# Optimization experiments

Hardware: AMD Instinct MI355X
Metric: run time of the kernel (lower is better)

## Reference

```python
import jax, jax.numpy as jnp
import numpy as np
from jax import lax

B, C, H, W = 8, 512, 16, 16
Di, N, R, K = 1024, 16, 32, 4  # d_inner, d_state, dt_rank, num scan directions
EPS = 1e-5


def _ln(x, g, b):
    mu = x.mean(-1, keepdims=True)
    var = ((x - mu) ** 2).mean(-1, keepdims=True)
    return (x - mu) * lax.rsqrt(var + EPS) * g + b


def _ss2d_core(xc, x_proj_w, dt_w, dt_b, A_logs, Ds):
    # xc: (b, Di, H, W) after depthwise conv + SiLU. 4-direction selective scan.
    b = xc.shape[0]
    L = H * W
    x_flat = xc.reshape(b, Di, L)
    x_wh = xc.transpose(0, 1, 3, 2).reshape(b, Di, L)
    x_hwwh = jnp.stack([x_flat, x_wh], 1)                  # (b,2,Di,L)
    xs = jnp.concatenate([x_hwwh, x_hwwh[..., ::-1]], 1)   # (b,K,Di,L)
    x_dbl = jnp.einsum('bkdl,kcd->bkcl', xs, x_proj_w)     # (b,K,R+2N,L)
    dts, Bs, Cs = x_dbl[:, :, :R], x_dbl[:, :, R:R + N], x_dbl[:, :, R + N:]
    dts = jnp.einsum('bkrl,kdr->bkdl', dts, dt_w)
    delta = jax.nn.softplus(dts + dt_b[None, :, :, None])  # (b,K,Di,L)
    A = -jnp.exp(A_logs).reshape(K, Di, N)                 # (K,Di,N)

    def step(h, inp):
        d, u, Bl, Cl = inp  # d,u:(b,K,Di)  Bl,Cl:(b,K,N)
        h = jnp.exp(d[..., None] * A) * h + (d * u)[..., None] * Bl[:, :, None, :]
        yl = jnp.einsum('bkdn,bkn->bkd', h, Cl)
        return h, yl

    inps = (delta.transpose(3, 0, 1, 2), xs.transpose(3, 0, 1, 2),
            Bs.transpose(3, 0, 1, 2), Cs.transpose(3, 0, 1, 2))
    h0 = jnp.zeros((b, K, Di, N), xc.dtype)
    _, ys = lax.scan(step, h0, inps)                       # (L,b,K,Di)
    ys = ys.transpose(1, 2, 3, 0) + xs * Ds.reshape(1, K, Di, 1)  # + D*u skip
    inv = ys[:, 2:4, :, ::-1]
    wh = ys[:, 1].reshape(b, Di, W, H).transpose(0, 1, 3, 2).reshape(b, Di, L)
    invwh = inv[:, 1].reshape(b, Di, W, H).transpose(0, 1, 3, 2).reshape(b, Di, L)
    y = ys[:, 0] + inv[:, 0] + wh + invwh                  # (b,Di,L)
    return y.transpose(0, 2, 1).reshape(b, H, W, Di)


def _conv_ffn(x, ffn_conv_w, bn_g, bn_b, bn_mean, bn_var, fc1_w, fc2_w):
    x = lax.conv_general_dilated(x, ffn_conv_w, (1, 1), [(1, 1), (1, 1)],
                                 dimension_numbers=('NCHW', 'OIHW', 'NCHW'))
    x = ((x - bn_mean[:, None, None]) * lax.rsqrt(bn_var + EPS)[:, None, None]
         * bn_g[:, None, None] + bn_b[:, None, None])
    x = jnp.clip(x, 0.0, 6.0)                              # ReLU6
    x = jnp.einsum('bchw,oc->bohw', x, fc1_w)              # 1x1 conv fc1
    x = jax.nn.gelu(x, approximate=False)
    return jnp.einsum('bchw,oc->bohw', x, fc2_w)           # 1x1 conv fc2


def _forward(x, y, ln1_g, ln1_b, in_proj_w, conv_w, conv_b, x_proj_w, dt_w,
             dt_b, A_logs, Ds, out_norm_g, out_norm_b, out_proj_w, ffn_conv_w,
             bn_g, bn_b, bn_mean, bn_var, fc1_w, fc2_w, lin1_w, lin1_b,
             lin2_w, lin2_b):
    # --- VSSBlock: LN -> SS2D -> residual ---
    x1 = x.transpose(0, 2, 3, 1)                           # (B,H,W,C)
    xn = _ln(x1, ln1_g, ln1_b)
    xz = jnp.einsum('bhwc,oc->bhwo', xn, in_proj_w)        # in_proj (no bias)
    xa, z = xz[..., :Di], xz[..., Di:]
    xc = xa.transpose(0, 3, 1, 2)                          # (B,Di,H,W)
    xc = lax.conv_general_dilated(xc, conv_w, (1, 1), [(1, 1), (1, 1)],
                                  feature_group_count=Di,
                                  dimension_numbers=('NCHW', 'OIHW', 'NCHW'))
    xc = jax.nn.silu(xc + conv_b[:, None, None])
    yc = _ss2d_core(xc, x_proj_w, dt_w, dt_b, A_logs, Ds)  # (B,H,W,Di)
    yc = _ln(yc, out_norm_g, out_norm_b) * jax.nn.silu(z)
    vss = x1 + jnp.einsum('bhwd,od->bhwo', yc, out_proj_w)
    # --- ConvFFN ---
    xm = _conv_ffn(vss.transpose(0, 3, 1, 2), ffn_conv_w, bn_g, bn_b, bn_mean,
                   bn_var, fc1_w, fc2_w)                   # (B,C,H,W)
    # --- channel attention: both pools are AdaptiveAvgPool2d(1), so max==avg ---
    pooled = y.mean(axis=(2, 3))                           # (B,C)
    lin = jax.nn.relu(pooled @ lin1_w.T + lin1_b) @ lin2_w.T + lin2_b
    gate = jax.nn.sigmoid(2.0 * lin)                       # linear_max + linear_avg
    return gate[:, :, None, None] * xm


def setup_inputs() -> dict:
    key = jax.random.key(0)
    ks = jax.random.split(key, 16)
    n = lambda i, shape, s=0.05: jax.random.normal(ks[i], shape, jnp.float32) * s
    return {
        'x': n(0, (B, C, H, W), 1.0),
        'y': n(1, (B, C, H, W), 1.0),
        'ln1_g': jnp.ones((C,), jnp.float32), 'ln1_b': jnp.zeros((C,), jnp.float32),
        'in_proj_w': n(2, (2 * Di, C)),
        'conv_w': n(3, (Di, 1, 3, 3), 0.2), 'conv_b': jnp.zeros((Di,), jnp.float32),
        'x_proj_w': n(4, (K, R + 2 * N, Di)),
        'dt_w': n(5, (K, Di, R), 0.1), 'dt_b': n(6, (K, Di), 0.1),
        'A_logs': n(7, (K * Di, N), 0.1), 'Ds': jnp.ones((K * Di,), jnp.float32),
        'out_norm_g': jnp.ones((Di,), jnp.float32), 'out_norm_b': jnp.zeros((Di,), jnp.float32),
        'out_proj_w': n(8, (C, Di)),
        'ffn_conv_w': n(9, (C, C, 3, 3)),
        'bn_g': jnp.ones((C,), jnp.float32), 'bn_b': jnp.zeros((C,), jnp.float32),
        'bn_mean': jnp.zeros((C,), jnp.float32), 'bn_var': jnp.ones((C,), jnp.float32),
        'fc1_w': n(10, (C, C)), 'fc2_w': n(11, (C, C)),
        'lin1_w': n(12, (C // 2, C)), 'lin1_b': jnp.zeros((C // 2,), jnp.float32),
        'lin2_w': n(13, (C, C // 2)), 'lin2_b': jnp.zeros((C,), jnp.float32),
    }


def reference(x, y, ln1_g, ln1_b, in_proj_w, conv_w, conv_b, x_proj_w, dt_w,
              dt_b, A_logs, Ds, out_norm_g, out_norm_b, out_proj_w, ffn_conv_w,
              bn_g, bn_b, bn_mean, bn_var, fc1_w, fc2_w, lin1_w, lin1_b,
              lin2_w, lin2_b):
    return _forward(x, y, ln1_g, ln1_b, in_proj_w, conv_w, conv_b, x_proj_w,
                    dt_w, dt_b, A_logs, Ds, out_norm_g, out_norm_b, out_proj_w,
                    ffn_conv_w, bn_g, bn_b, bn_mean, bn_var, fc1_w, fc2_w,
                    lin1_w, lin1_b, lin2_w, lin2_b)
```

## Files before the change

### kernel.cpp

```cpp
#include <hip/hip_runtime.h>
#include <hip/hip_bf16.h>
#include <math.h>

#define DEV_INLINE __device__ __forceinline__

constexpr int B_ = 8, C_ = 512, L_ = 256;
constexpr float EPS_ = 1e-5f;

typedef __attribute__((ext_vector_type(8))) short bf16x8;
typedef __attribute__((ext_vector_type(4))) float f32x4;

DEV_INLINE int lmap1(int l) { return ((l & 15) << 4) | (l >> 4); }
DEV_INLINE float sigmoidf_(float x) { return 1.f / (1.f + __expf(-x)); }
DEV_INLINE float siluf_(float x) { return x * sigmoidf_(x); }

DEV_INLINE unsigned pk2(float a, float b) {
    __hip_bfloat16 x = __float2bfloat16(a), y = __float2bfloat16(b);
    unsigned short ux = *reinterpret_cast<unsigned short*>(&x);
    unsigned short uy = *reinterpret_cast<unsigned short*>(&y);
    return ((unsigned)uy << 16) | ux;
}

__global__ __launch_bounds__(256) void k_pool(const float* __restrict__ y, float* __restrict__ pooled) {
    int bc = blockIdx.x;
    int t = threadIdx.x;
    __shared__ float red[256];
    red[t] = y[bc * 256 + t];
    __syncthreads();
    for (int s = 128; s > 0; s >>= 1) { if (t < s) red[t] += red[t + s]; __syncthreads(); }
    if (t == 0) pooled[bc] = red[0] * (1.f / 256.f);
}

__global__ __launch_bounds__(256) void k_gate(const float* __restrict__ pooled,
                                              const float* __restrict__ lin1_w, const float* __restrict__ lin1_b,
                                              const float* __restrict__ lin2_w, const float* __restrict__ lin2_b,
                                              float* __restrict__ gate) {
    int b = blockIdx.x;
    int t = threadIdx.x;
    __shared__ float p[512];
    __shared__ float h1[256];
    p[t] = pooled[b * 512 + t];
    p[t + 256] = pooled[b * 512 + t + 256];
    __syncthreads();
    float s = lin1_b[t];
    for (int c = 0; c < 512; ++c) s = fmaf(p[c], lin1_w[t * 512 + c], s);
    h1[t] = fmaxf(s, 0.f);
    __syncthreads();
    #pragma unroll
    for (int cc = 0; cc < 2; ++cc) {
        int c = t + cc * 256;
        float s2 = lin2_b[c];
        for (int j = 0; j < 256; ++j) s2 = fmaf(h1[j], lin2_w[c * 256 + j], s2);
        gate[b * 512 + c] = sigmoidf_(2.f * s2);
    }
}

__global__ __launch_bounds__(256) void k_ln(const float* __restrict__ x, const float* __restrict__ g,
                                            const float* __restrict__ bta, float* __restrict__ xn) {
    int pos = blockIdx.x;
    int b = pos >> 8, l = pos & 255;
    int t = threadIdx.x;
    float v0 = x[(b * C_ + t) * L_ + l];
    float v1 = x[(b * C_ + t + 256) * L_ + l];
    __shared__ float red[256];
    red[t] = v0 + v1;
    __syncthreads();
    for (int s = 128; s > 0; s >>= 1) { if (t < s) red[t] += red[t + s]; __syncthreads(); }
    float mu = red[0] * (1.f / 512.f);
    __syncthreads();
    float d0 = v0 - mu, d1 = v1 - mu;
    red[t] = d0 * d0 + d1 * d1;
    __syncthreads();
    for (int s = 128; s > 0; s >>= 1) { if (t < s) red[t] += red[t + s]; __syncthreads(); }
    float rs = rsqrtf(red[0] * (1.f / 512.f) + EPS_);
    xn[pos * C_ + t] = d0 * rs * g[t] + bta[t];
    xn[pos * C_ + t + 256] = d1 * rs * g[t + 256] + bta[t + 256];
}

__global__ __launch_bounds__(256) void k_wcast5(const float* __restrict__ ip, const float* __restrict__ xp,
                                                const float* __restrict__ op, const float* __restrict__ f1,
                                                const float* __restrict__ f2, __hip_bfloat16* __restrict__ dst) {
    size_t e = ((size_t)blockIdx.x * 256 + threadIdx.x) * 4;
    const float* src; size_t off;
    if (e < 1048576) { src = ip; off = e; }
    else if (e < 1310720) { src = xp; off = e - 1048576; }
    else if (e < 1835008) { src = op; off = e - 1310720; }
    else if (e < 2097152) { src = f1; off = e - 1835008; }
    else { src = f2; off = e - 2097152; }
    float4 v = *(const float4*)(src + off);
    uint2 o; o.x = pk2(v.x, v.y); o.y = pk2(v.z, v.w);
    *(uint2*)(dst + e) = o;
}

enum { M_INPROJ = 0, M_XDBL = 1, M_OUTPROJ = 2, M_FC1 = 3, M_FC2 = 4 };

template <int MODE>
__global__ __launch_bounds__(256) void gemm_mfma(const float* __restrict__ Af, const __hip_bfloat16* __restrict__ Wb,
                                                 float* __restrict__ O, float* __restrict__ O2,
                                                 const float* __restrict__ AUX, __hip_bfloat16* __restrict__ Ob) {
    constexpr int KK = (MODE == M_XDBL || MODE == M_OUTPROJ) ? 1024 : 512;
    __shared__ short Asm[64 * 32];
    __shared__ short Bsm[64 * 32];
    const int t = threadIdx.x;
    const int lane = t & 63, wv = t >> 6;
    int m0, n0 = 0, kdir = 0, bq = 0;
    if constexpr (MODE == M_XDBL) { m0 = blockIdx.x * 64; kdir = blockIdx.y; }
    else if constexpr (MODE == M_FC2) { bq = blockIdx.x >> 3; m0 = (blockIdx.x & 7) * 64; n0 = blockIdx.y * 64; }
    else { m0 = blockIdx.x * 64; n0 = blockIdx.y * 64; }

    const int r_ = t >> 2, kq = t & 3;
    const int skey = (r_ >> 1) & 3;
    uint4* adst = (uint4*)(Asm + r_ * 32) + (kq ^ skey);
    uint4* bdst = (uint4*)(Bsm + r_ * 32) + (kq ^ skey);

    const float* arowf = nullptr;
    const __hip_bfloat16* arowb = nullptr;
    if constexpr (MODE == M_INPROJ) arowf = Af + (size_t)(m0 + r_) * 512 + kq * 8;
    else if constexpr (MODE == M_XDBL) {
        int m = m0 + r_; int b = m >> 8, l = m & 255;
        int lm = (kdir < 2) ? l : 255 - l;
        arowf = Af + (size_t)((b * 2 + (kdir & 1)) * 256 + lm) * 1024 + kq * 8;
    } else if constexpr (MODE == M_OUTPROJ) arowf = Af + (size_t)(m0 + r_) * 1024 + kq * 8;
    else if constexpr (MODE == M_FC1) arowf = Af + (size_t)(m0 + r_) * 512 + kq * 8;
    else arowb = Wb + (size_t)(m0 + r_) * 512 + kq * 8;

    const __hip_bfloat16* browb = nullptr;
    const float* browf = nullptr;
    if constexpr (MODE == M_INPROJ) browb = Wb + (size_t)(n0 + r_) * 512 + kq * 8;
    else if constexpr (MODE == M_XDBL) browb = Wb + (size_t)(kdir * 64 + r_) * 1024 + kq * 8;
    else if constexpr (MODE == M_OUTPROJ) browb = Wb + (size_t)(n0 + r_) * 1024 + kq * 8;
    else if constexpr (MODE == M_FC1) browb = Wb + (size_t)(n0 + r_) * 512 + kq * 8;
    else browf = Af + (size_t)(bq * 256 + n0 + r_) * 512 + kq * 8;

    f32x4 acc[4];
    #pragma unroll
    for (int nf = 0; nf < 4; ++nf) acc[nf] = (f32x4){0.f, 0.f, 0.f, 0.f};

    for (int k0 = 0; k0 < KK; k0 += 32) {
        __syncthreads();
        if constexpr (MODE == M_FC2) {
            *adst = *(const uint4*)(arowb + k0);
            float4 u0 = *(const float4*)(browf + k0);
            float4 u1 = *(const float4*)(browf + k0 + 4);
            uint4 pk; pk.x = pk2(u0.x, u0.y); pk.y = pk2(u0.z, u0.w); pk.z = pk2(u1.x, u1.y); pk.w = pk2(u1.z, u1.w);
            *bdst = pk;
        } else {
            float4 u0 = *(const float4*)(arowf + k0);
            float4 u1 = *(const float4*)(arowf + k0 + 4);
            uint4 pk; pk.x = pk2(u0.x, u0.y); pk.y = pk2(u0.z, u0.w); pk.z = pk2(u1.x, u1.y); pk.w = pk2(u1.z, u1.w);
            *adst = pk;
            *bdst = *(const uint4*)(browb + k0);
        }
        __syncthreads();
        int mrow = wv * 16 + (lane & 15);
        int ks = lane >> 4;
        bf16x8 af = *(const bf16x8*)(Asm + mrow * 32 + ((ks ^ ((mrow >> 1) & 3)) * 8));
        #pragma unroll
        for (int nf = 0; nf < 4; ++nf) {
            int nrow = nf * 16 + (lane & 15);
            bf16x8 bfv = *(const bf16x8*)(Bsm + nrow * 32 + ((ks ^ ((nrow >> 1) & 3)) * 8));
            acc[nf] = __builtin_amdgcn_mfma_f32_16x16x32_bf16(af, bfv, acc[nf], 0, 0, 0);
        }
    }

    const int mlb = (lane >> 4) * 4, nl = lane & 15;
    #pragma unroll
    for (int nf = 0; nf < 4; ++nf) {
        #pragma unroll
        for (int j = 0; j < 4; ++j) {
            float v = acc[nf][j];
            int m_loc = wv * 16 + mlb + j;
            int n_loc = nf * 16 + nl;
            if constexpr (MODE == M_INPROJ) {
                int m = m0 + m_loc, n = n0 + n_loc;
                if (n0 < 1024) O[(size_t)m * 1024 + n] = v;
                else O2[(size_t)m * 1024 + (n - 1024)] = v;
            } else if constexpr (MODE == M_XDBL) {
                int m = m0 + m_loc; int b = m >> 8, l = m & 255;
                O[((size_t)(b * 4 + kdir) * 256 + l) * 64 + n_loc] = v;
            } else if constexpr (MODE == M_OUTPROJ) {
                int m = m0 + m_loc, n = n0 + n_loc; int b = m >> 8, l = m & 255;
                float f = AUX[((size_t)b * 512 + n) * 256 + l] + v;
                Ob[(size_t)m * 512 + n] = __float2bfloat16(f);
            } else if constexpr (MODE == M_FC1) {
                int m = m0 + m_loc, n = n0 + n_loc;
                O[(size_t)m * 512 + n] = 0.5f * v * (1.f + erff(v * 0.70710678118f));
            } else {
                int c = m0 + m_loc, n = n0 + n_loc;
                O[((size_t)(bq * 512 + c)) * 256 + n] = v * AUX[bq * 512 + c];
            }
        }
    }
}

__global__ __launch_bounds__(256) void k_dwconv2(const float* __restrict__ xa, const float* __restrict__ cw,
                                                 const float* __restrict__ cb, float* __restrict__ xs_t) {
    int pos = blockIdx.x;
    int b = pos >> 8, l = pos & 255;
    int h = l >> 4, w = l & 15;
    int t = threadIdx.x;
    int d = t * 4;
    float wv[36];
    {
        const float4* cp = (const float4*)(cw + (size_t)d * 9);
        #pragma unroll
        for (int j = 0; j < 9; ++j) { float4 v = cp[j]; wv[j*4] = v.x; wv[j*4+1] = v.y; wv[j*4+2] = v.z; wv[j*4+3] = v.w; }
    }
    float4 bias = *(const float4*)(cb + d);
    float a0 = bias.x, a1 = bias.y, a2 = bias.z, a3 = bias.w;
    #pragma unroll
    for (int ky = -1; ky <= 1; ++ky) {
        int hh = h + ky;
        if ((unsigned)hh >= 16u) continue;
        #pragma unroll
        for (int kx = -1; kx <= 1; ++kx) {
            int ww = w + kx;
            if ((unsigned)ww >= 16u) continue;
            float4 v = *(const float4*)(xa + (size_t)(b * 256 + hh * 16 + ww) * 1024 + d);
            int tap = (ky + 1) * 3 + (kx + 1);
            a0 = fmaf(v.x, wv[0 * 9 + tap], a0);
            a1 = fmaf(v.y, wv[1 * 9 + tap], a1);
            a2 = fmaf(v.z, wv[2 * 9 + tap], a2);
            a3 = fmaf(v.w, wv[3 * 9 + tap], a3);
        }
    }
    float4 o; o.x = siluf_(a0); o.y = siluf_(a1); o.z = siluf_(a2); o.w = siluf_(a3);
    *(float4*)(xs_t + ((size_t)(b * 2 + 0) * 256 + l) * 1024 + d) = o;
    *(float4*)(xs_t + ((size_t)(b * 2 + 1) * 256 + lmap1(l)) * 1024 + d) = o;
}

__global__ __launch_bounds__(128) void k_scan2(const float* __restrict__ xs_t, const float* __restrict__ x_dbl,
                                               const float* __restrict__ dt_w, const float* __restrict__ dt_b,
                                               const float* __restrict__ A_logs, const float* __restrict__ Ds,
                                               float* __restrict__ ys_t) {
    const int bk = blockIdx.x >> 5;
    const int b = bk >> 2, k = bk & 3;
    const int d0 = (blockIdx.x & 31) * 32;
    const int t = threadIdx.x;
    const int ch = t >> 2, nq = t & 3;
    const int d = d0 + ch;

    __shared__ float xds[32][64];
    __shared__ float us[32][32];

    float wr[8];
    #pragma unroll
    for (int j = 0; j < 8; ++j) wr[j] = dt_w[(size_t)(k * 1024 + d) * 32 + nq * 8 + j];
    const float dtb = dt_b[k * 1024 + d];
    float An[4];
    #pragma unroll
    for (int i = 0; i < 4; ++i) An[i] = -__expf(A_logs[(size_t)(k * 1024 + d) * 16 + nq * 4 + i]);
    const float Dv = Ds[k * 1024 + d];
    float h[4] = {0.f, 0.f, 0.f, 0.f};

    const float* xs_base = xs_t + (size_t)(b * 2 + (k & 1)) * 256 * 1024 + d0;
    const float* xd_base = x_dbl + (size_t)(b * 4 + k) * 256 * 64;
    float* ys_base = ys_t + (size_t)(b * 4 + k) * 256 * 1024 + d;
    const bool rev = (k >= 2);

    for (int l0 = 0; l0 < 256; l0 += 32) {
        __syncthreads();
        #pragma unroll
        for (int i = t; i < 512; i += 128) {
            int row = i >> 4, c4 = i & 15;
            *(float4*)&xds[row][c4 * 4] = *(const float4*)(xd_base + (size_t)(l0 + row) * 64 + c4 * 4);
        }
        #pragma unroll
        for (int i = t; i < 1024; i += 128) {
            int row = i >> 5, c = i & 31;
            int lm = rev ? (255 - (l0 + row)) : (l0 + row);
            us[row][c] = xs_base[(size_t)lm * 1024 + c];
        }
        __syncthreads();
        #pragma unroll 2
        for (int li = 0; li < 32; ++li) {
            const float* xd = &xds[li][0];
            float draw = 0.f;
            #pragma unroll
            for (int j = 0; j < 8; ++j) draw = fmaf(xd[nq * 8 + j], wr[j], draw);
            draw += __shfl_xor(draw, 1);
            draw += __shfl_xor(draw, 2);
            draw += dtb;
            float delta = (draw > 20.f) ? draw : __logf(1.f + __expf(draw));
            float u = us[li][ch];
            float du = delta * u;
            float yv = 0.f;
            #pragma unroll
            for (int i = 0; i < 4; ++i) {
                float Bn = xd[32 + nq * 4 + i], Cn = xd[48 + nq * 4 + i];
                h[i] = fmaf(__expf(delta * An[i]), h[i], du * Bn);
                yv = fmaf(h[i], Cn, yv);
            }
            yv += __shfl_xor(yv, 1);
            yv += __shfl_xor(yv, 2);
            if (nq == 0) ys_base[(size_t)(l0 + li) * 1024] = yv + u * Dv;
        }
    }
}

__global__ __launch_bounds__(256) void k_combine(const float* __restrict__ ys_t, const float* __restrict__ z,
                                                 const float* __restrict__ g, const float* __restrict__ bb,
                                                 float* __restrict__ yc) {
    int pos = blockIdx.x;
    int b = pos >> 8, l = pos & 255;
    int t = threadIdx.x;
    int lw = lmap1(l);
    const float* r0 = ys_t + (size_t)((b * 4 + 0) * 256 + l) * 1024;
    const float* r1 = ys_t + (size_t)((b * 4 + 1) * 256 + lw) * 1024;
    const float* r2 = ys_t + (size_t)((b * 4 + 2) * 256 + (255 - l)) * 1024;
    const float* r3 = ys_t + (size_t)((b * 4 + 3) * 256 + (255 - lw)) * 1024;
    float v[4];
    float psum = 0.f;
    #pragma unroll
    for (int q = 0; q < 4; ++q) {
        int d = t + q * 256;
        v[q] = r0[d] + r1[d] + r2[d] + r3[d];
        psum += v[q];
    }
    __shared__ float red[256];
    red[t] = psum;
    __syncthreads();
    for (int s = 128; s > 0; s >>= 1) { if (t < s) red[t] += red[t + s]; __syncthreads(); }
    float mu = red[0] * (1.f / 1024.f);
    __syncthreads();
    float p2 = 0.f;
    #pragma unroll
    for (int q = 0; q < 4; ++q) { float dd = v[q] - mu; p2 += dd * dd; }
    red[t] = p2;
    __syncthreads();
    for (int s = 128; s > 0; s >>= 1) { if (t < s) red[t] += red[t + s]; __syncthreads(); }
    float rs = rsqrtf(red[0] * (1.f / 1024.f) + EPS_);
    #pragma unroll
    for (int q = 0; q < 4; ++q) {
        int d = t + q * 256;
        float zn = z[(size_t)pos * 1024 + d];
        yc[(size_t)pos * 1024 + d] = ((v[q] - mu) * rs * g[d] + bb[d]) * siluf_(zn);
    }
}

__global__ __launch_bounds__(256) void k_wcast(const float* __restrict__ w, __hip_bfloat16* __restrict__ wt) {
    int gid = blockIdx.x * 256 + threadIdx.x;
    const float* src = w + (size_t)gid * 9;
    #pragma unroll
    for (int tap = 0; tap < 9; ++tap) wt[(size_t)tap * 262144 + gid] = __float2bfloat16(src[tap]);
}

__global__ __launch_bounds__(256) void k_conv2m(const __hip_bfloat16* __restrict__ vssb,
                                                const __hip_bfloat16* __restrict__ wt,
                                                float* __restrict__ convp) {
    __shared__ short Asm[18 * 18 * 32];
    __shared__ short Bsm[9 * 64 * 32];
    const int b = blockIdx.x, co0 = blockIdx.y * 64, split = blockIdx.z;
    const int t = threadIdx.x;
    const int lane = t & 63, wid = t >> 6;
    const int wcol = lane & 15, slot = lane >> 4;

    f32x4 acc[4][4];
    #pragma unroll
    for (int r = 0; r < 4; ++r)
        #pragma unroll
        for (int g = 0; g < 4; ++g) acc[r][g] = (f32x4){0.f, 0.f, 0.f, 0.f};

    for (int ch = 0; ch < 4; ++ch) {
        const int ci0 = split * 128 + ch * 32;
        __syncthreads();
        for (int i = t; i < 324; i += 256) {
            int row = i / 18, col = i - row * 18;
            uint4 v0 = {0,0,0,0}, v1 = {0,0,0,0}, v2 = {0,0,0,0}, v3 = {0,0,0,0};
            if (row >= 1 && row <= 16 && col >= 1 && col <= 16) {
                const uint4* src = (const uint4*)(vssb + ((size_t)(b * 256 + (row - 1) * 16 + (col - 1)) * 512 + ci0));
                v0 = src[0]; v1 = src[1]; v2 = src[2]; v3 = src[3];
            }
            uint4* dst = (uint4*)(Asm + i * 32);
            int key = (col >> 1) & 3;
            dst[0 ^ key] = v0; dst[1 ^ key] = v1; dst[2 ^ key] = v2; dst[3 ^ key] = v3;
        }
        for (int i = t; i < 576; i += 256) {
            int tap = i >> 6, col = i & 63;
            const uint4* src = (const uint4*)(wt + ((size_t)(tap * 512 + co0 + col) * 512 + ci0));
            uint4* dst = (uint4*)(Bsm + i * 32);
            int key = (col >> 1) & 3;
            dst[0 ^ key] = src[0]; dst[1 ^ key] = src[1]; dst[2 ^ key] = src[2]; dst[3 ^ key] = src[3];
        }
        __syncthreads();
        #pragma unroll
        for (int tap = 0; tap < 9; ++tap) {
            const int ky = tap / 3, kx = tap - ky * 3;
            bf16x8 af[4], bfr[4];
            #pragma unroll
            for (int r = 0; r < 4; ++r) {
                int crow = wid * 4 + r + ky;
                int ccol = wcol + kx;
                int s2 = slot ^ ((ccol >> 1) & 3);
                af[r] = *(const bf16x8*)(Asm + ((crow * 18 + ccol) * 32 + s2 * 8));
            }
            #pragma unroll
            for (int g = 0; g < 4; ++g) {
                int col = g * 16 + wcol;
                int s2 = slot ^ ((col >> 1) & 3);
                bfr[g] = *(const bf16x8*)(Bsm + ((tap * 64 + col) * 32 + s2 * 8));
            }
            #pragma unroll
            for (int r = 0; r < 4; ++r)
                #pragma unroll
                for (int g = 0; g < 4; ++g)
                    acc[r][g] = __builtin_amdgcn_mfma_f32_16x16x32_bf16(af[r], bfr[g], acc[r][g], 0, 0, 0);
        }
    }
    float* base = convp + (size_t)split * 1048576 + (size_t)b * 512 * 256;
    #pragma unroll
    for (int r = 0; r < 4; ++r) {
        int h = wid * 4 + r;
        #pragma unroll
        for (int g = 0; g < 4; ++g) {
            int co = co0 + g * 16 + wcol;
            *(f32x4*)(base + (size_t)co * 256 + h * 16 + slot * 4) = acc[r][g];
        }
    }
}

__global__ __launch_bounds__(256) void k_convred2(const float* __restrict__ convp,
                                                  const float* __restrict__ bn_g, const float* __restrict__ bn_b,
                                                  const float* __restrict__ bn_mean, const float* __restrict__ bn_var,
                                                  float* __restrict__ t1) {
    int b = blockIdx.x >> 7, cb = (blockIdx.x >> 3) & 15, pb = blockIdx.x & 7;
    int co0 = cb * 32, pos0 = pb * 32;
    int t = threadIdx.x;
    int ti = t >> 5, tj = t & 31;
    __shared__ float tile[32][33];
    #pragma unroll
    for (int r = 0; r < 4; ++r) {
        int co = co0 + ti + r * 8;
        size_t idx = ((size_t)b * 512 + co) * 256 + pos0 + tj;
        float s = convp[idx] + convp[idx + 1048576] + convp[idx + 2097152] + convp[idx + 3145728];
        float o = (s - bn_mean[co]) * rsqrtf(bn_var[co] + EPS_) * bn_g[co] + bn_b[co];
        tile[ti + r * 8][tj] = fminf(fmaxf(o, 0.f), 6.f);
    }
    __syncthreads();
    #pragma unroll
    for (int r = 0; r < 4; ++r) {
        int pos = pos0 + ti + r * 8;
        t1[((size_t)b * 256 + pos) * 512 + co0 + tj] = tile[tj][ti + r * 8];
    }
}

extern "C" void kernel_launch(void* const* d_in, const int* in_sizes, int n_in,
                              void* d_out, int out_size, void* d_ws, size_t ws_size,
                              hipStream_t stream) {
    const float* x = (const float*)d_in[0];
    const float* y = (const float*)d_in[1];
    const float* ln1_g = (const float*)d_in[2];
    const float* ln1_b = (const float*)d_in[3];
    const float* in_proj_w = (const float*)d_in[4];
    const float* conv_w = (const float*)d_in[5];
    const float* conv_b = (const float*)d_in[6];
    const float* x_proj_w = (const float*)d_in[7];
    const float* dt_w = (const float*)d_in[8];
    const float* dt_b = (const float*)d_in[9];
    const float* A_logs = (const float*)d_in[10];
    const float* Ds = (const float*)d_in[11];
    const float* out_norm_g = (const float*)d_in[12];
    const float* out_norm_b = (const float*)d_in[13];
    const float* out_proj_w = (const float*)d_in[14];
    const float* ffn_conv_w = (const float*)d_in[15];
    const float* bn_g = (const float*)d_in[16];
    const float* bn_b = (const float*)d_in[17];
    const float* bn_mean = (const float*)d_in[18];
    const float* bn_var = (const float*)d_in[19];
    const float* fc1_w = (const float*)d_in[20];
    const float* fc2_w = (const float*)d_in[21];
    const float* lin1_w = (const float*)d_in[22];
    const float* lin1_b = (const float*)d_in[23];
    const float* lin2_w = (const float*)d_in[24];
    const float* lin2_b = (const float*)d_in[25];
    float* out = (float*)d_out;

    char* ws = (char*)d_ws;
    size_t off = 0;
    auto alloc = [&](size_t nf) { float* p = (float*)(ws + off); off += nf * sizeof(float); return p; };
    float* xn    = alloc(2048u * 512);
    float* xa    = alloc(2048u * 1024);
    float* z     = alloc(2048u * 1024);
    float* xs_t  = alloc(2u * 2048 * 1024);
    float* x_dbl = alloc(8u * 4 * 256 * 64);
    float* ys_t  = alloc(4u * 2048 * 1024);
    float* wb    = alloc(2359296u / 2);
    float* pooled = alloc(4096);
    float* gate   = alloc(4096);

    float* yc = xa;
    float* t1 = xs_t;
    float* t2 = xs_t + 2048u * 512;
    __hip_bfloat16* vssb = (__hip_bfloat16*)xn;
    __hip_bfloat16* w_t  = (__hip_bfloat16*)z;
    float* convp = ys_t;
    __hip_bfloat16* inprojb = (__hip_bfloat16*)wb;
    __hip_bfloat16* xprojb  = inprojb + 1048576;
    __hip_bfloat16* outprojb = xprojb + 262144;
    __hip_bfloat16* fc1b = outprojb + 524288;
    __hip_bfloat16* fc2b = fc1b + 262144;

    k_wcast5<<<2304, 256, 0, stream>>>(in_proj_w, x_proj_w, out_proj_w, fc1_w, fc2_w, inprojb);
    k_pool<<<4096, 256, 0, stream>>>(y, pooled);
    k_gate<<<8, 256, 0, stream>>>(pooled, lin1_w, lin1_b, lin2_w, lin2_b, gate);
    k_ln<<<2048, 256, 0, stream>>>(x, ln1_g, ln1_b, xn);
    gemm_mfma<M_INPROJ><<<dim3(32, 32), 256, 0, stream>>>(xn, inprojb, xa, z, nullptr, nullptr);
    k_dwconv2<<<2048, 256, 0, stream>>>(xa, conv_w, conv_b, xs_t);
    gemm_mfma<M_XDBL><<<dim3(32, 4), 256, 0, stream>>>(xs_t, xprojb, x_dbl, nullptr, nullptr, nullptr);
    k_scan2<<<1024, 128, 0, stream>>>(xs_t, x_dbl, dt_w, dt_b, A_logs, Ds, ys_t);
    k_combine<<<2048, 256, 0, stream>>>(ys_t, z, out_norm_g, out_norm_b, yc);
    k_wcast<<<1024, 256, 0, stream>>>(ffn_conv_w, w_t);
    gemm_mfma<M_OUTPROJ><<<dim3(32, 8), 256, 0, stream>>>(yc, outprojb, nullptr, nullptr, x, vssb);
    k_conv2m<<<dim3(8, 8, 4), 256, 0, stream>>>(vssb, w_t, convp);
    k_convred2<<<1024, 256, 0, stream>>>(convp, bn_g, bn_b, bn_mean, bn_var, t1);
    gemm_mfma<M_FC1><<<dim3(32, 8), 256, 0, stream>>>(t1, fc1b, t2, nullptr, nullptr, nullptr);
    gemm_mfma<M_FC2><<<dim3(64, 4), 256, 0, stream>>>(t2, fc2b, out, nullptr, gate, nullptr);
}
```

Measured before the change: 294.9 us.

## Precompute delta via MFMA GEMM and simplify scan to register-prefetched loop

The dt projection plus softplus is moved out of the scan into a new bf16 MFMA GEMM mode that writes delta into the ys buffer. The scan kernel then reads delta in place, drops its shared-memory staging and per-step dot product, and prefetches the next step's operands into registers. This trades an extra kernel launch and a full delta write/read pass through global memory, plus bf16 rounding of dt_w and the dt inputs, for a shorter serial per-step critical path in the scan.

```diff
diff --git a/kernel.cpp b/kernel.cpp
--- a/kernel.cpp
+++ b/kernel.cpp
@@ -79,26 +79,28 @@
 
 __global__ __launch_bounds__(256) void k_wcast5(const float* __restrict__ ip, const float* __restrict__ xp,
                                                 const float* __restrict__ op, const float* __restrict__ f1,
-                                                const float* __restrict__ f2, __hip_bfloat16* __restrict__ dst) {
+                                                const float* __restrict__ f2, const float* __restrict__ dtw,
+                                                __hip_bfloat16* __restrict__ dst) {
     size_t e = ((size_t)blockIdx.x * 256 + threadIdx.x) * 4;
     const float* src; size_t off;
     if (e < 1048576) { src = ip; off = e; }
     else if (e < 1310720) { src = xp; off = e - 1048576; }
     else if (e < 1835008) { src = op; off = e - 1310720; }
     else if (e < 2097152) { src = f1; off = e - 1835008; }
-    else { src = f2; off = e - 2097152; }
+    else if (e < 2359296) { src = f2; off = e - 2097152; }
+    else { src = dtw; off = e - 2359296; }
     float4 v = *(const float4*)(src + off);
     uint2 o; o.x = pk2(v.x, v.y); o.y = pk2(v.z, v.w);
     *(uint2*)(dst + e) = o;
 }
 
-enum { M_INPROJ = 0, M_XDBL = 1, M_OUTPROJ = 2, M_FC1 = 3, M_FC2 = 4 };
+enum { M_INPROJ = 0, M_XDBL = 1, M_OUTPROJ = 2, M_FC1 = 3, M_FC2 = 4, M_DELTA = 5 };
 
 template <int MODE>
 __global__ __launch_bounds__(256) void gemm_mfma(const float* __restrict__ Af, const __hip_bfloat16* __restrict__ Wb,
                                                  float* __restrict__ O, float* __restrict__ O2,
                                                  const float* __restrict__ AUX, __hip_bfloat16* __restrict__ Ob) {
-    constexpr int KK = (MODE == M_XDBL || MODE == M_OUTPROJ) ? 1024 : 512;
+    constexpr int KK = (MODE == M_XDBL || MODE == M_OUTPROJ) ? 1024 : (MODE == M_DELTA) ? 32 : 512;
     __shared__ short Asm[64 * 32];
     __shared__ short Bsm[64 * 32];
     const int t = threadIdx.x;
@@ -107,6 +109,7 @@
     if constexpr (MODE == M_XDBL) { m0 = blockIdx.x * 64; kdir = blockIdx.y; }
     else if constexpr (MODE == M_FC2) { bq = blockIdx.x >> 3; m0 = (blockIdx.x & 7) * 64; n0 = blockIdx.y * 64; }
     else { m0 = blockIdx.x * 64; n0 = blockIdx.y * 64; }
+    const int kdel = (m0 >> 8) & 3;
 
     const int r_ = t >> 2, kq = t & 3;
     const int skey = (r_ >> 1) & 3;
@@ -122,6 +125,7 @@
         arowf = Af + (size_t)((b * 2 + (kdir & 1)) * 256 + lm) * 1024 + kq * 8;
     } else if constexpr (MODE == M_OUTPROJ) arowf = Af + (size_t)(m0 + r_) * 1024 + kq * 8;
     else if constexpr (MODE == M_FC1) arowf = Af + (size_t)(m0 + r_) * 512 + kq * 8;
+    else if constexpr (MODE == M_DELTA) arowf = Af + (size_t)(m0 + r_) * 64 + kq * 8;
     else arowb = Wb + (size_t)(m0 + r_) * 512 + kq * 8;
 
     const __hip_bfloat16* browb = nullptr;
@@ -130,6 +134,7 @@
     else if constexpr (MODE == M_XDBL) browb = Wb + (size_t)(kdir * 64 + r_) * 1024 + kq * 8;
     else if constexpr (MODE == M_OUTPROJ) browb = Wb + (size_t)(n0 + r_) * 1024 + kq * 8;
     else if constexpr (MODE == M_FC1) browb = Wb + (size_t)(n0 + r_) * 512 + kq * 8;
+    else if constexpr (MODE == M_DELTA) browb = Wb + ((size_t)(kdel * 1024 + n0 + r_)) * 32 + kq * 8;
     else browf = Af + (size_t)(bq * 256 + n0 + r_) * 512 + kq * 8;
 
     f32x4 acc[4];
@@ -185,6 +190,11 @@
             } else if constexpr (MODE == M_FC1) {
                 int m = m0 + m_loc, n = n0 + n_loc;
                 O[(size_t)m * 512 + n] = 0.5f * v * (1.f + erff(v * 0.70710678118f));
+            } else if constexpr (MODE == M_DELTA) {
+                int m = m0 + m_loc, n = n0 + n_loc;
+                float v2 = v + AUX[kdel * 1024 + n];
+                float dlt = (v2 > 20.f) ? v2 : __logf(1.f + __expf(v2));
+                O[(size_t)m * 1024 + n] = dlt;
             } else {
                 int c = m0 + m_loc, n = n0 + n_loc;
                 O[((size_t)(bq * 512 + c)) * 256 + n] = v * AUX[bq * 512 + c];
@@ -229,72 +239,50 @@
     *(float4*)(xs_t + ((size_t)(b * 2 + 1) * 256 + lmap1(l)) * 1024 + d) = o;
 }
 
-__global__ __launch_bounds__(128) void k_scan2(const float* __restrict__ xs_t, const float* __restrict__ x_dbl,
-                                               const float* __restrict__ dt_w, const float* __restrict__ dt_b,
+__global__ __launch_bounds__(256) void k_scan3(const float* __restrict__ xs_t, const float* __restrict__ x_dbl,
                                                const float* __restrict__ A_logs, const float* __restrict__ Ds,
                                                float* __restrict__ ys_t) {
-    const int bk = blockIdx.x >> 5;
+    const int g = blockIdx.x * 256 + threadIdx.x;
+    const int nq = g & 3;
+    const int chain = g >> 2;
+    const int d = chain & 1023, bk = chain >> 10;
     const int b = bk >> 2, k = bk & 3;
-    const int d0 = (blockIdx.x & 31) * 32;
-    const int t = threadIdx.x;
-    const int ch = t >> 2, nq = t & 3;
-    const int d = d0 + ch;
-
-    __shared__ float xds[32][64];
-    __shared__ float us[32][32];
-
-    float wr[8];
-    #pragma unroll
-    for (int j = 0; j < 8; ++j) wr[j] = dt_w[(size_t)(k * 1024 + d) * 32 + nq * 8 + j];
-    const float dtb = dt_b[k * 1024 + d];
+
     float An[4];
     #pragma unroll
     for (int i = 0; i < 4; ++i) An[i] = -__expf(A_logs[(size_t)(k * 1024 + d) * 16 + nq * 4 + i]);
     const float Dv = Ds[k * 1024 + d];
-    float h[4] = {0.f, 0.f, 0.f, 0.f};
-
-    const float* xs_base = xs_t + (size_t)(b * 2 + (k & 1)) * 256 * 1024 + d0;
-    const float* xd_base = x_dbl + (size_t)(b * 4 + k) * 256 * 64;
-    float* ys_base = ys_t + (size_t)(b * 4 + k) * 256 * 1024 + d;
     const bool rev = (k >= 2);
 
-    for (int l0 = 0; l0 < 256; l0 += 32) {
-        __syncthreads();
-        #pragma unroll
-        for (int i = t; i < 512; i += 128) {
-            int row = i >> 4, c4 = i & 15;
-            *(float4*)&xds[row][c4 * 4] = *(const float4*)(xd_base + (size_t)(l0 + row) * 64 + c4 * 4);
-        }
-        #pragma unroll
-        for (int i = t; i < 1024; i += 128) {
-            int row = i >> 5, c = i & 31;
-            int lm = rev ? (255 - (l0 + row)) : (l0 + row);
-            us[row][c] = xs_base[(size_t)lm * 1024 + c];
-        }
-        __syncthreads();
-        #pragma unroll 2
-        for (int li = 0; li < 32; ++li) {
-            const float* xd = &xds[li][0];
-            float draw = 0.f;
-            #pragma unroll
-            for (int j = 0; j < 8; ++j) draw = fmaf(xd[nq * 8 + j], wr[j], draw);
-            draw += __shfl_xor(draw, 1);
-            draw += __shfl_xor(draw, 2);
-            draw += dtb;
-            float delta = (draw > 20.f) ? draw : __logf(1.f + __expf(draw));
-            float u = us[li][ch];
-            float du = delta * u;
-            float yv = 0.f;
-            #pragma unroll
-            for (int i = 0; i < 4; ++i) {
-                float Bn = xd[32 + nq * 4 + i], Cn = xd[48 + nq * 4 + i];
-                h[i] = fmaf(__expf(delta * An[i]), h[i], du * Bn);
-                yv = fmaf(h[i], Cn, yv);
-            }
-            yv += __shfl_xor(yv, 1);
-            yv += __shfl_xor(yv, 2);
-            if (nq == 0) ys_base[(size_t)(l0 + li) * 1024] = yv + u * Dv;
-        }
+    const float* up = xs_t + ((size_t)(b * 2 + (k & 1)) * 256 + (rev ? 255 : 0)) * 1024 + d;
+    const ptrdiff_t ustr = rev ? -1024 : 1024;
+    const float* xp = x_dbl + (size_t)bk * 256 * 64 + 32 + nq * 4;
+    float* yp = ys_t + (size_t)bk * 256 * 1024 + d;
+
+    float h0 = 0.f, h1 = 0.f, h2 = 0.f, h3 = 0.f;
+    float dl = yp[0];
+    float u = up[0];
+    float4 Bv = *(const float4*)(xp);
+    float4 Cv = *(const float4*)(xp + 16);
+
+    for (int l = 0; l < 256; ++l) {
+        int lp = (l < 255) ? l + 1 : 255;
+        float dl_n = yp[(size_t)lp * 1024];
+        float u_n = up[(ptrdiff_t)lp * ustr];
+        float4 Bv_n = *(const float4*)(xp + lp * 64);
+        float4 Cv_n = *(const float4*)(xp + lp * 64 + 16);
+
+        float du = dl * u;
+        float yv;
+        h0 = fmaf(__expf(dl * An[0]), h0, du * Bv.x); yv = h0 * Cv.x;
+        h1 = fmaf(__expf(dl * An[1]), h1, du * Bv.y); yv = fmaf(h1, Cv.y, yv);
+        h2 = fmaf(__expf(dl * An[2]), h2, du * Bv.z); yv = fmaf(h2, Cv.z, yv);
+        h3 = fmaf(__expf(dl * An[3]), h3, du * Bv.w); yv = fmaf(h3, Cv.w, yv);
+        yv += __shfl_xor(yv, 1);
+        yv += __shfl_xor(yv, 2);
+        if (nq == 0) yp[(size_t)l * 1024] = yv + u * Dv;
+
+        dl = dl_n; u = u_n; Bv = Bv_n; Cv = Cv_n;
     }
 }
 
@@ -484,7 +472,7 @@
     float* xs_t  = alloc(2u * 2048 * 1024);
     float* x_dbl = alloc(8u * 4 * 256 * 64);
     float* ys_t  = alloc(4u * 2048 * 1024);
-    float* wb    = alloc(2359296u / 2);
+    float* wb    = alloc(1245184);
     float* pooled = alloc(4096);
     float* gate   = alloc(4096);
 
@@ -499,15 +487,17 @@
     __hip_bfloat16* outprojb = xprojb + 262144;
     __hip_bfloat16* fc1b = outprojb + 524288;
     __hip_bfloat16* fc2b = fc1b + 262144;
-
-    k_wcast5<<<2304, 256, 0, stream>>>(in_proj_w, x_proj_w, out_proj_w, fc1_w, fc2_w, inprojb);
+    __hip_bfloat16* dtwb = fc2b + 262144;
+
+    k_wcast5<<<2432, 256, 0, stream>>>(in_proj_w, x_proj_w, out_proj_w, fc1_w, fc2_w, dt_w, inprojb);
     k_pool<<<4096, 256, 0, stream>>>(y, pooled);
     k_gate<<<8, 256, 0, stream>>>(pooled, lin1_w, lin1_b, lin2_w, lin2_b, gate);
     k_ln<<<2048, 256, 0, stream>>>(x, ln1_g, ln1_b, xn);
     gemm_mfma<M_INPROJ><<<dim3(32, 32), 256, 0, stream>>>(xn, inprojb, xa, z, nullptr, nullptr);
     k_dwconv2<<<2048, 256, 0, stream>>>(xa, conv_w, conv_b, xs_t);
     gemm_mfma<M_XDBL><<<dim3(32, 4), 256, 0, stream>>>(xs_t, xprojb, x_dbl, nullptr, nullptr, nullptr);
-    k_scan2<<<1024, 128, 0, stream>>>(xs_t, x_dbl, dt_w, dt_b, A_logs, Ds, ys_t);
+    gemm_mfma<M_DELTA><<<dim3(128, 16), 256, 0, stream>>>(x_dbl, dtwb, ys_t, nullptr, dt_b, nullptr);
+    k_scan3<<<512, 256, 0, stream>>>(xs_t, x_dbl, A_logs, Ds, ys_t);
     k_combine<<<2048, 256, 0, stream>>>(ys_t, z, out_norm_g, out_norm_b, yc);
     k_wcast<<<1024, 256, 0, stream>>>(ffn_conv_w, w_t);
     gemm_mfma<M_OUTPROJ><<<dim3(32, 8), 256, 0, stream>>>(yc, outprojb, nullptr, nullptr, x, vssb);
```

New measurement: 316.5 us. 7.3% more time.
